# Performance work log

Hardware: AMD Instinct MI355X
Metric: run time of the kernel (lower is better)

Reference implementation:

```python
import jax, jax.numpy as jnp
import numpy as np

D_MODEL = 1024
NHEAD = 16
WINDOW = 128


def setup_inputs() -> dict:
    key = jax.random.key(0)
    ks = jax.random.split(key, 7)
    B, L, D = 4, 4096, D_MODEL
    s = 0.02
    return {
        "q": jax.random.normal(ks[0], (B, L, D), jnp.float32),
        "k": jax.random.normal(ks[1], (B, L, D), jnp.float32),
        "v": jax.random.normal(ks[2], (B, L, D), jnp.float32),
        "in_proj_w": jax.random.normal(ks[3], (3 * D, D), jnp.float32) * s,
        "in_proj_b": jnp.zeros((3 * D,), jnp.float32),
        "out_w": jax.random.normal(ks[4], (D, D), jnp.float32) * s,
        "out_b": jnp.zeros((D,), jnp.float32),
    }


def reference(q, k, v, in_proj_w, in_proj_b, out_w, out_b):
    B, L, D = q.shape
    H, W = NHEAD, WINDOW
    hd = D // H
    nW = L // W
    Wq, Wk, Wv = in_proj_w[:D], in_proj_w[D:2 * D], in_proj_w[2 * D:]
    bq, bk, bv = in_proj_b[:D], in_proj_b[D:2 * D], in_proj_b[2 * D:]
    # shared per-window projections (same weights every window, as in nn.MultiheadAttention)
    qp = (q @ Wq.T + bq).reshape(B, nW, W, H, hd)
    kp = (k @ Wk.T + bk).reshape(B, nW, W, H, hd)
    vp = (v @ Wv.T + bv).reshape(B, nW, W, H, hd)
    scale = 1.0 / np.sqrt(hd).astype(np.float32)
    # block-diagonal attention: scores only within each window n
    scores = jnp.einsum("bnqhd,bnkhd->bnhqk", qp, kp) * scale  # [B,nW,H,W,W]
    attn = jax.nn.softmax(scores, axis=-1)
    out = jnp.einsum("bnhqk,bnkhd->bnqhd", attn, vp).reshape(B, L, D)
    return out @ out_w.T + out_b
```

## Files before the change

kernel.cpp:

```cpp
#include <hip/hip_runtime.h>

#define M_TOK 16384
#define DM    1024

typedef __bf16 bf16x8 __attribute__((ext_vector_type(8)));
typedef float  f32x4  __attribute__((ext_vector_type(4)));
typedef unsigned short us8 __attribute__((ext_vector_type(8)));
typedef unsigned short us4 __attribute__((ext_vector_type(4)));

__device__ __forceinline__ unsigned short f2bf(float f) {
    unsigned u = __float_as_uint(f);
    u += 0x7FFFu + ((u >> 16) & 1u);
    return (unsigned short)(u >> 16);
}

__device__ __forceinline__ void gl2lds16(const unsigned short* g, unsigned short* l) {
    __builtin_amdgcn_global_load_lds(
        (const __attribute__((address_space(1))) unsigned int*)g,
        (__attribute__((address_space(3))) unsigned int*)l, 16, 0, 0);
}

__global__ __launch_bounds__(256) void conv_f2b(
    const float* __restrict__ src, unsigned short* __restrict__ dst, int n8)
{
    int i = blockIdx.x * blockDim.x + threadIdx.x;
    int stride = gridDim.x * blockDim.x;
    for (; i < n8; i += stride) {
        const float4* s = (const float4*)(src + (size_t)i * 8);
        float4 a = s[0], b = s[1];
        us8 o;
        o[0] = f2bf(a.x); o[1] = f2bf(a.y); o[2] = f2bf(a.z); o[3] = f2bf(a.w);
        o[4] = f2bf(b.x); o[5] = f2bf(b.y); o[6] = f2bf(b.z); o[7] = f2bf(b.w);
        *(us8*)(dst + (size_t)i * 8) = o;
    }
}

#define PIPE_WAIT8() asm volatile("s_waitcnt vmcnt(8)" ::: "memory")
#define PIPE_WAIT0() asm volatile("s_waitcnt vmcnt(0)" ::: "memory")

#define STAGE(G_, k0_, Lb_)                                                  \
    _Pragma("unroll")                                                        \
    for (int j = 0; j < 4; ++j) {                                            \
        int p = tid + j * 512;                                               \
        int kkp = p >> 10, rem = p & 1023;                                   \
        int r = rem >> 2, cp = rem & 3;                                      \
        int cl = cp ^ ((r >> 1) & 3);                                        \
        gl2lds16((G_) + (size_t)r * DM + (k0_) + kkp * 32 + cl * 8,          \
                 (Lb_) + p * 8);                                             \
    }

#define COMPUTE(bi_)                                                         \
    _Pragma("unroll")                                                        \
    for (int kk = 0; kk < 2; ++kk) {                                         \
        bf16x8 af[8], bb[4];                                                 \
        _Pragma("unroll")                                                    \
        for (int mi = 0; mi < 8; ++mi)                                       \
            af[mi] = *(const bf16x8*)(smem[bi_] + kk * 8192 + sA + mi * 512);\
        _Pragma("unroll")                                                    \
        for (int ni = 0; ni < 4; ++ni)                                       \
            bb[ni] = *(const bf16x8*)(smem[bi_] + kk * 8192 + sB + ni * 512);\
        __builtin_amdgcn_s_setprio(1);                                       \
        _Pragma("unroll")                                                    \
        for (int mi = 0; mi < 8; ++mi)                                       \
            _Pragma("unroll")                                                \
            for (int ni = 0; ni < 4; ++ni)                                   \
                acc[mi][ni] = __builtin_amdgcn_mfma_f32_16x16x32_bf16(       \
                    af[mi], bb[ni], acc[mi][ni], 0, 0, 0);                   \
        __builtin_amdgcn_s_setprio(0);                                       \
    }

#define GEMM256_CORE(A_, B_)                                                 \
    __shared__ unsigned short smem[2][32768];                    \
    const int tid = threadIdx.x, lane = tid & 63, wv = tid >> 6;             \
    const int wm = wv >> 2, wn = wv & 3;                                     \
    const int lrow = lane & 15, qd = lane >> 4;                              \
    const int orig = blockIdx.y * 4 + blockIdx.x;     \
    const int swz  = (orig & 7) * 32 + (orig >> 3);                          \
    const int mbase = (swz >> 2) * 256, nbase = (swz & 3) * 256;             \
    const unsigned short* Ab = (A_) + (size_t)mbase * DM;                    \
    const unsigned short* Bb = (B_) + (size_t)nbase * DM;                    \
              \
    const int sA = (qd ^ ((lrow >> 1) & 3)) * 8 + (wm * 128 + lrow) * 32;    \
    const int sB = (qd ^ ((lrow >> 1) & 3)) * 8 + (wn * 64 + lrow) * 32      \
                   + 16384;                                                  \
    f32x4 acc[8][4] = {};                                                    \
                                                \
    STAGE(Ab, 0, smem[0]);  STAGE(Bb, 0, smem[0] + 16384);                   \
    STAGE(Ab, 64, smem[1]); STAGE(Bb, 64, smem[1] + 16384);                  \
    PIPE_WAIT8();                                                            \
    __builtin_amdgcn_s_barrier();                                            \
    __builtin_amdgcn_sched_barrier(0);                                       \
    _Pragma("unroll 1")                                                      \
    for (int t = 0; t < 16; t += 2) {                                        \
        COMPUTE(0);                                                          \
        __builtin_amdgcn_sched_barrier(0);                                   \
        __builtin_amdgcn_s_barrier();       \
        if (t + 2 < 16) {                                                    \
            STAGE(Ab, (t + 2) * 64, smem[0]);                                \
            STAGE(Bb, (t + 2) * 64, smem[0] + 16384);                        \
            PIPE_WAIT8();                               \
        } else {                                                             \
            PIPE_WAIT0();                                    \
        }                                                                    \
        __builtin_amdgcn_s_barrier();                                        \
        __builtin_amdgcn_sched_barrier(0);                                   \
        COMPUTE(1);                                                          \
        __builtin_amdgcn_sched_barrier(0);                                   \
        __builtin_amdgcn_s_barrier();                                        \
        if (t + 3 < 16) {                                                    \
            STAGE(Ab, (t + 3) * 64, smem[1]);                                \
            STAGE(Bb, (t + 3) * 64, smem[1] + 16384);                        \
            PIPE_WAIT8();                               \
        } else if (t + 2 < 16) {                                             \
            PIPE_WAIT0();                                                    \
        }                                                                    \
        __builtin_amdgcn_s_barrier();                                        \
        __builtin_amdgcn_sched_barrier(0);                                   \
    }

__global__ __launch_bounds__(512, 2) void gemm256_qkv(
    const unsigned short* __restrict__ A, const unsigned short* __restrict__ W,
    const float* __restrict__ bias, unsigned short* __restrict__ C, int z)
{
    GEMM256_CORE(A, W)
    if (z <= 1) {
        #pragma unroll
        for (int ni = 0; ni < 4; ++ni) {
            int gc = nbase + wn * 64 + ni * 16 + lrow;
            int h = gc >> 6, dh = gc & 63;
            float bv = bias[gc];
            #pragma unroll
            for (int mi = 0; mi < 8; ++mi) {
                int gr0 = mbase + wm * 128 + mi * 16 + qd * 4;
                int b = gr0 >> 12;
                #pragma unroll
                for (int r = 0; r < 4; ++r) {
                    int tok = (gr0 + r) & 4095;
                    C[(((size_t)b * 16 + h) * 4096 + tok) * 64 + dh] =
                        f2bf(acc[mi][ni][r] + bv);
                }
            }
        }
    } else {
        #pragma unroll
        for (int ni = 0; ni < 4; ++ni) {
            int gc = nbase + wn * 64 + ni * 16 + lrow;
            int h = gc >> 6, dh = gc & 63;
            float bv = bias[gc];
            #pragma unroll
            for (int mi = 0; mi < 8; ++mi) {
                int gr0 = mbase + wm * 128 + mi * 16 + qd * 4;
                int b = gr0 >> 12, tok = gr0 & 4095;
                us4 pk;
                #pragma unroll
                for (int r = 0; r < 4; ++r) pk[r] = f2bf(acc[mi][ni][r] + bv);
                *(us4*)(C + (((size_t)b * 16 + h) * 64 + dh) * 4096 + tok) = pk;
            }
        }
    }
}

__global__ __launch_bounds__(512, 2) void gemm256_out(
    const unsigned short* __restrict__ A, const unsigned short* __restrict__ W,
    const float* __restrict__ bias, float* __restrict__ out)
{
    GEMM256_CORE(A, W)
    #pragma unroll
    for (int ni = 0; ni < 4; ++ni) {
        int gc = nbase + wn * 64 + ni * 16 + lrow;
        float bv = bias[gc];
        #pragma unroll
        for (int mi = 0; mi < 8; ++mi) {
            int gr0 = mbase + wm * 128 + mi * 16 + qd * 4;
            #pragma unroll
            for (int r = 0; r < 4; ++r)
                out[(size_t)(gr0 + r) * DM + gc] = acc[mi][ni][r] + bv;
        }
    }
}

__global__ __launch_bounds__(256) void attn_v2(
    const unsigned short* __restrict__ qh, const unsigned short* __restrict__ kh,
    const unsigned short* __restrict__ vt, unsigned short* __restrict__ aout)
{
    const int gid = blockIdx.x;
    const int h  = gid & 15;
    const int wi = (gid >> 4) & 31;
    const int b  = gid >> 9;
    const int bh = b * 16 + h;

    const unsigned short* Qp = qh + ((size_t)bh * 4096 + wi * 128) * 64;
    const unsigned short* Kp = kh + ((size_t)bh * 4096 + wi * 128) * 64;
    const unsigned short* Vp = vt + (size_t)bh * 64 * 4096 + wi * 128;

    const int tid = threadIdx.x, lane = tid & 63, wv = tid >> 6;
    const int lrow = lane & 15, qd = lane >> 4, kof = qd * 8;

    __shared__ unsigned short Ps[128 * 136];

    f32x4 acc[2][8] = {};
    #pragma unroll
    for (int ki = 0; ki < 2; ++ki) {
        bf16x8 a0 = *(const bf16x8*)(Qp + (wv * 32 +  0 + lrow) * 64 + ki * 32 + kof);
        bf16x8 a1 = *(const bf16x8*)(Qp + (wv * 32 + 16 + lrow) * 64 + ki * 32 + kof);
        #pragma unroll
        for (int ni = 0; ni < 8; ++ni) {
            bf16x8 bb = *(const bf16x8*)(Kp + (ni * 16 + lrow) * 64 + ki * 32 + kof);
            acc[0][ni] = __builtin_amdgcn_mfma_f32_16x16x32_bf16(a0, bb, acc[0][ni], 0, 0, 0);
            acc[1][ni] = __builtin_amdgcn_mfma_f32_16x16x32_bf16(a1, bb, acc[1][ni], 0, 0, 0);
        }
    }

    const float scale = 0.125f;
    #pragma unroll
    for (int mi = 0; mi < 2; ++mi) {
        #pragma unroll
        for (int r = 0; r < 4; ++r) {
            float sc[8];
            float mx = -3.4e38f;
            #pragma unroll
            for (int ni = 0; ni < 8; ++ni) { sc[ni] = acc[mi][ni][r] * scale; mx = fmaxf(mx, sc[ni]); }
            mx = fmaxf(mx, __shfl_xor(mx, 1));
            mx = fmaxf(mx, __shfl_xor(mx, 2));
            mx = fmaxf(mx, __shfl_xor(mx, 4));
            mx = fmaxf(mx, __shfl_xor(mx, 8));
            float sum = 0.f;
            #pragma unroll
            for (int ni = 0; ni < 8; ++ni) { sc[ni] = __expf(sc[ni] - mx); sum += sc[ni]; }
            sum += __shfl_xor(sum, 1);
            sum += __shfl_xor(sum, 2);
            sum += __shfl_xor(sum, 4);
            sum += __shfl_xor(sum, 8);
            float inv = 1.0f / sum;
            #pragma unroll
            for (int ni = 0; ni < 8; ++ni) acc[mi][ni][r] = sc[ni] * inv;
        }
    }

    #pragma unroll
    for (int mi = 0; mi < 2; ++mi)
        #pragma unroll
        for (int ni = 0; ni < 8; ++ni)
            #pragma unroll
            for (int r = 0; r < 4; ++r)
                Ps[(wv * 32 + mi * 16 + qd * 4 + r) * 136 + ni * 16 + lrow] =
                    f2bf(acc[mi][ni][r]);

    f32x4 o[2][4] = {};
    #pragma unroll
    for (int kj = 0; kj < 4; ++kj) {
        bf16x8 a0 = *(const bf16x8*)(Ps + (wv * 32 +  0 + lrow) * 136 + kj * 32 + kof);
        bf16x8 a1 = *(const bf16x8*)(Ps + (wv * 32 + 16 + lrow) * 136 + kj * 32 + kof);
        #pragma unroll
        for (int nd = 0; nd < 4; ++nd) {
            bf16x8 bb = *(const bf16x8*)(Vp + (size_t)(nd * 16 + lrow) * 4096 + kj * 32 + kof);
            o[0][nd] = __builtin_amdgcn_mfma_f32_16x16x32_bf16(a0, bb, o[0][nd], 0, 0, 0);
            o[1][nd] = __builtin_amdgcn_mfma_f32_16x16x32_bf16(a1, bb, o[1][nd], 0, 0, 0);
        }
    }

    #pragma unroll
    for (int mi = 0; mi < 2; ++mi)
        #pragma unroll
        for (int nd = 0; nd < 4; ++nd)
            #pragma unroll
            for (int r = 0; r < 4; ++r) {
                int R = wv * 32 + mi * 16 + qd * 4 + r;
                int c = h * 64 + nd * 16 + lrow;
                aout[(size_t)(b * 4096 + wi * 128 + R) * DM + c] = f2bf(o[mi][nd][r]);
            }
}

__global__ __launch_bounds__(256) void gemm_qkv_v1(
    const float* __restrict__ qin, const float* __restrict__ kin,
    const float* __restrict__ vin, const float* __restrict__ ipw,
    const float* __restrict__ ipb, unsigned short* __restrict__ qkv)
{
    __shared__ unsigned short As[128 * 40];
    __shared__ unsigned short Ws[128 * 40];
    const int z = blockIdx.z;
    const float* A  = (z == 0) ? qin : ((z == 1) ? kin : vin);
    const float* Wp = ipw + (size_t)z * DM * DM;
    const float* bp = ipb + z * DM;
    unsigned short* Cp = qkv + (size_t)z * M_TOK * DM;
    const int mbase = blockIdx.y * 128, nbase = blockIdx.x * 128;
    const int tid = threadIdx.x, lane = tid & 63, wv = tid >> 6;
    const int wrow = (wv >> 1) * 64, wcol = (wv & 1) * 64;
    const int lrow = lane & 15, kof = (lane >> 4) * 8;
    const int srow = tid >> 3, sc4 = tid & 7;
    f32x4 acc[4][4] = {};
    for (int ks = 0; ks < 32; ++ks) {
        const int k0 = ks * 32;
        __syncthreads();
        #pragma unroll
        for (int it = 0; it < 4; ++it) {
            int row = it * 32 + srow;
            float4 av = *(const float4*)(A  + (size_t)(mbase + row) * DM + k0 + sc4 * 4);
            float4 wf = *(const float4*)(Wp + (size_t)(nbase + row) * DM + k0 + sc4 * 4);
            us4 ap, wp4;
            ap[0] = f2bf(av.x); ap[1] = f2bf(av.y); ap[2] = f2bf(av.z); ap[3] = f2bf(av.w);
            wp4[0] = f2bf(wf.x); wp4[1] = f2bf(wf.y); wp4[2] = f2bf(wf.z); wp4[3] = f2bf(wf.w);
            *(us4*)(As + row * 40 + sc4 * 4) = ap;
            *(us4*)(Ws + row * 40 + sc4 * 4) = wp4;
        }
        __syncthreads();
        bf16x8 af[4], bfr[4];
        #pragma unroll
        for (int i = 0; i < 4; ++i) af[i]  = *(const bf16x8*)(As + (wrow + i * 16 + lrow) * 40 + kof);
        #pragma unroll
        for (int i = 0; i < 4; ++i) bfr[i] = *(const bf16x8*)(Ws + (wcol + i * 16 + lrow) * 40 + kof);
        #pragma unroll
        for (int i = 0; i < 4; ++i)
            #pragma unroll
            for (int j = 0; j < 4; ++j)
                acc[i][j] = __builtin_amdgcn_mfma_f32_16x16x32_bf16(af[i], bfr[j], acc[i][j], 0, 0, 0);
    }
    #pragma unroll
    for (int j = 0; j < 4; ++j) {
        int gc = nbase + wcol + j * 16 + lrow;
        float bv = bp[gc];
        #pragma unroll
        for (int i = 0; i < 4; ++i) {
            int gr0 = mbase + wrow + i * 16 + (lane >> 4) * 4;
            #pragma unroll
            for (int r = 0; r < 4; ++r)
                Cp[(size_t)(gr0 + r) * DM + gc] = f2bf(acc[i][j][r] + bv);
        }
    }
}

__global__ __launch_bounds__(256) void gemm_out_v1(
    const unsigned short* __restrict__ x, const float* __restrict__ ow,
    const float* __restrict__ ob, float* __restrict__ out)
{
    __shared__ unsigned short As[128 * 40];
    __shared__ unsigned short Ws[128 * 40];
    const int mbase = blockIdx.y * 128, nbase = blockIdx.x * 128;
    const int tid = threadIdx.x, lane = tid & 63, wv = tid >> 6;
    const int wrow = (wv >> 1) * 64, wcol = (wv & 1) * 64;
    const int lrow = lane & 15, kof = (lane >> 4) * 8;
    const int srow = tid >> 3, sc4 = tid & 7;
    f32x4 acc[4][4] = {};
    for (int ks = 0; ks < 32; ++ks) {
        const int k0 = ks * 32;
        __syncthreads();
        #pragma unroll
        for (int it = 0; it < 4; ++it) {
            int row = it * 32 + srow;
            us4 av = *(const us4*)(x + (size_t)(mbase + row) * DM + k0 + sc4 * 4);
            float4 wf = *(const float4*)(ow + (size_t)(nbase + row) * DM + k0 + sc4 * 4);
            us4 wp4;
            wp4[0] = f2bf(wf.x); wp4[1] = f2bf(wf.y); wp4[2] = f2bf(wf.z); wp4[3] = f2bf(wf.w);
            *(us4*)(As + row * 40 + sc4 * 4) = av;
            *(us4*)(Ws + row * 40 + sc4 * 4) = wp4;
        }
        __syncthreads();
        bf16x8 af[4], bfr[4];
        #pragma unroll
        for (int i = 0; i < 4; ++i) af[i]  = *(const bf16x8*)(As + (wrow + i * 16 + lrow) * 40 + kof);
        #pragma unroll
        for (int i = 0; i < 4; ++i) bfr[i] = *(const bf16x8*)(Ws + (wcol + i * 16 + lrow) * 40 + kof);
        #pragma unroll
        for (int i = 0; i < 4; ++i)
            #pragma unroll
            for (int j = 0; j < 4; ++j)
                acc[i][j] = __builtin_amdgcn_mfma_f32_16x16x32_bf16(af[i], bfr[j], acc[i][j], 0, 0, 0);
    }
    #pragma unroll
    for (int j = 0; j < 4; ++j) {
        int gc = nbase + wcol + j * 16 + lrow;
        float bv = ob[gc];
        #pragma unroll
        for (int i = 0; i < 4; ++i) {
            int gr0 = mbase + wrow + i * 16 + (lane >> 4) * 4;
            #pragma unroll
            for (int r = 0; r < 4; ++r)
                out[(size_t)(gr0 + r) * DM + gc] = acc[i][j][r] + bv;
        }
    }
}

__global__ __launch_bounds__(256) void attn_win_v1(
    const unsigned short* __restrict__ qkv, unsigned short* __restrict__ aout)
{
    const unsigned short* qp = qkv;
    const unsigned short* kp = qkv + (size_t)M_TOK * DM;
    const unsigned short* vp = qkv + 2 * (size_t)M_TOK * DM;
    const int gid = blockIdx.x;
    const int h = gid & 15, wi = (gid >> 4) & 31, b = gid >> 9;
    const size_t rowbase = (size_t)b * 4096 + (size_t)wi * 128;
    const int tid = threadIdx.x, lane = tid & 63, wv = tid >> 6;
    const int lrow = lane & 15, kof = (lane >> 4) * 8;
    __shared__ unsigned short sm[27136];
    unsigned short* Qs = sm;
    unsigned short* Ks = sm + 9216;
    unsigned short* Vt = sm + 18432;
    unsigned short* Ps = sm;
    {
        const int seg = tid & 7;
        #pragma unroll
        for (int it = 0; it < 4; ++it) {
            int r = it * 32 + (tid >> 3);
            size_t g = (rowbase + r) * DM + h * 64 + seg * 8;
            *(int4*)(Qs + r * 72 + seg * 8) = *(const int4*)(qp + g);
            *(int4*)(Ks + r * 72 + seg * 8) = *(const int4*)(kp + g);
        }
        #pragma unroll
        for (int it = 0; it < 4; ++it) {
            int j = tid & 127;
            int sg = it * 2 + (tid >> 7);
            us8 vv = *(const us8*)(vp + (rowbase + j) * DM + h * 64 + sg * 8);
            #pragma unroll
            for (int d = 0; d < 8; ++d) Vt[(sg * 8 + d) * 136 + j] = vv[d];
        }
    }
    __syncthreads();
    f32x4 acc[2][8] = {};
    #pragma unroll
    for (int ki = 0; ki < 2; ++ki) {
        bf16x8 a0 = *(const bf16x8*)(Qs + (wv * 32 +  0 + lrow) * 72 + ki * 32 + kof);
        bf16x8 a1 = *(const bf16x8*)(Qs + (wv * 32 + 16 + lrow) * 72 + ki * 32 + kof);
        #pragma unroll
        for (int ni = 0; ni < 8; ++ni) {
            bf16x8 bb = *(const bf16x8*)(Ks + (ni * 16 + lrow) * 72 + ki * 32 + kof);
            acc[0][ni] = __builtin_amdgcn_mfma_f32_16x16x32_bf16(a0, bb, acc[0][ni], 0, 0, 0);
            acc[1][ni] = __builtin_amdgcn_mfma_f32_16x16x32_bf16(a1, bb, acc[1][ni], 0, 0, 0);
        }
    }
    const float scale = 0.125f;
    #pragma unroll
    for (int mi = 0; mi < 2; ++mi) {
        #pragma unroll
        for (int r = 0; r < 4; ++r) {
            float sc[8];
            float mx = -3.4e38f;
            #pragma unroll
            for (int ni = 0; ni < 8; ++ni) { sc[ni] = acc[mi][ni][r] * scale; mx = fmaxf(mx, sc[ni]); }
            mx = fmaxf(mx, __shfl_xor(mx, 1)); mx = fmaxf(mx, __shfl_xor(mx, 2));
            mx = fmaxf(mx, __shfl_xor(mx, 4)); mx = fmaxf(mx, __shfl_xor(mx, 8));
            float sum = 0.f;
            #pragma unroll
            for (int ni = 0; ni < 8; ++ni) { sc[ni] = __expf(sc[ni] - mx); sum += sc[ni]; }
            sum += __shfl_xor(sum, 1); sum += __shfl_xor(sum, 2);
            sum += __shfl_xor(sum, 4); sum += __shfl_xor(sum, 8);
            float inv = 1.0f / sum;
            #pragma unroll
            for (int ni = 0; ni < 8; ++ni) acc[mi][ni][r] = sc[ni] * inv;
        }
    }
    __syncthreads();
    #pragma unroll
    for (int mi = 0; mi < 2; ++mi)
        #pragma unroll
        for (int ni = 0; ni < 8; ++ni)
            #pragma unroll
            for (int r = 0; r < 4; ++r)
                Ps[(wv * 32 + mi * 16 + (lane >> 4) * 4 + r) * 136 + ni * 16 + lrow] =
                    f2bf(acc[mi][ni][r]);
    __syncthreads();
    f32x4 o[2][4] = {};
    #pragma unroll
    for (int kj = 0; kj < 4; ++kj) {
        bf16x8 a0 = *(const bf16x8*)(Ps + (wv * 32 +  0 + lrow) * 136 + kj * 32 + kof);
        bf16x8 a1 = *(const bf16x8*)(Ps + (wv * 32 + 16 + lrow) * 136 + kj * 32 + kof);
        #pragma unroll
        for (int nd = 0; nd < 4; ++nd) {
            bf16x8 bb = *(const bf16x8*)(Vt + (nd * 16 + lrow) * 136 + kj * 32 + kof);
            o[0][nd] = __builtin_amdgcn_mfma_f32_16x16x32_bf16(a0, bb, o[0][nd], 0, 0, 0);
            o[1][nd] = __builtin_amdgcn_mfma_f32_16x16x32_bf16(a1, bb, o[1][nd], 0, 0, 0);
        }
    }
    #pragma unroll
    for (int mi = 0; mi < 2; ++mi)
        #pragma unroll
        for (int nd = 0; nd < 4; ++nd)
            #pragma unroll
            for (int r = 0; r < 4; ++r) {
                int R = wv * 32 + mi * 16 + (lane >> 4) * 4 + r;
                int c = h * 64 + nd * 16 + lrow;
                aout[(rowbase + R) * DM + c] = f2bf(o[mi][nd][r]);
            }
}

extern "C" void kernel_launch(void* const* d_in, const int* in_sizes, int n_in,
                              void* d_out, int out_size, void* d_ws, size_t ws_size,
                              hipStream_t stream) {
    const float* q   = (const float*)d_in[0];
    const float* k   = (const float*)d_in[1];
    const float* v   = (const float*)d_in[2];
    const float* ipw = (const float*)d_in[3];
    const float* ipb = (const float*)d_in[4];
    const float* ow  = (const float*)d_in[5];
    const float* ob  = (const float*)d_in[6];
    float* out = (float*)d_out;

    const size_t MD = (size_t)M_TOK * DM;
    const size_t WW = (size_t)DM * DM;
    const size_t need = (4 * MD + 3 * WW) * 2;

    if (ws_size >= need) {
        unsigned short* X   = (unsigned short*)d_ws;
        unsigned short* qh  = X + MD;
        unsigned short* kh  = X + 2 * MD;
        unsigned short* vtb = X + 3 * MD;
        unsigned short* Wb  = X + 4 * MD;
        unsigned short* aout = X;
        unsigned short* OwB  = Wb;

        conv_f2b<<<1536, 256, 0, stream>>>(ipw, Wb, (int)(3 * WW / 8));
        conv_f2b<<<8192, 256, 0, stream>>>(q, X, (int)(MD / 8));
        gemm256_qkv<<<dim3(4, 64), 512, 0, stream>>>(X, Wb, ipb, qh, 0);
        conv_f2b<<<8192, 256, 0, stream>>>(k, X, (int)(MD / 8));
        gemm256_qkv<<<dim3(4, 64), 512, 0, stream>>>(X, Wb + WW, ipb + DM, kh, 1);
        conv_f2b<<<8192, 256, 0, stream>>>(v, X, (int)(MD / 8));
        gemm256_qkv<<<dim3(4, 64), 512, 0, stream>>>(X, Wb + 2 * WW, ipb + 2 * DM, vtb, 2);
        conv_f2b<<<512, 256, 0, stream>>>(ow, OwB, (int)(WW / 8));
        attn_v2<<<2048, 256, 0, stream>>>(qh, kh, vtb, aout);
        gemm256_out<<<dim3(4, 64), 512, 0, stream>>>(aout, OwB, ob, out);
    } else {
        unsigned short* qkv = (unsigned short*)d_ws;
        const size_t qkv_elems = 3 * MD;
        const size_t need_full = (qkv_elems + MD) * 2;
        unsigned short* aout = (ws_size >= need_full) ? qkv + qkv_elems : qkv;
        gemm_qkv_v1<<<dim3(8, 128, 3), 256, 0, stream>>>(q, k, v, ipw, ipb, qkv);
        attn_win_v1<<<2048, 256, 0, stream>>>(qkv, aout);
        gemm_out_v1<<<dim3(8, 128), 256, 0, stream>>>(aout, ow, ob, out);
    }
}
```

Baseline: 531.9 us.

## Restructure GEMM LDS pipeline into 4-slot ring of 32-wide K stages

Replaces the double-buffered 64-wide K staging, which used two barriers per half-step, with a four-slot ring of 32-wide K slices. Each iteration issues loads two slices ahead and needs only one waitcnt plus one barrier. This should cut barrier count and keep more global-to-LDS loads in flight alongside the MFMA work. LDS use stays at 128KB. The tighter single-barrier scheme risks races, because the slot being written (kh+2) is the one read two iterations earlier.

```diff
diff --git a/kernel.cpp b/kernel.cpp
--- a/kernel.cpp
+++ b/kernel.cpp
@@ -35,30 +35,53 @@
     }
 }
 
-#define PIPE_WAIT8() asm volatile("s_waitcnt vmcnt(8)" ::: "memory")
-#define PIPE_WAIT0() asm volatile("s_waitcnt vmcnt(0)" ::: "memory")
-
-#define STAGE(G_, k0_, Lb_)                                                  \
-    _Pragma("unroll")                                                        \
-    for (int j = 0; j < 4; ++j) {                                            \
-        int p = tid + j * 512;                                               \
-        int kkp = p >> 10, rem = p & 1023;                                   \
-        int r = rem >> 2, cp = rem & 3;                                      \
-        int cl = cp ^ ((r >> 1) & 3);                                        \
-        gl2lds16((G_) + (size_t)r * DM + (k0_) + kkp * 32 + cl * 8,          \
-                 (Lb_) + p * 8);                                             \
-    }
-
-#define COMPUTE(bi_)                                                         \
-    _Pragma("unroll")                                                        \
-    for (int kk = 0; kk < 2; ++kk) {                                         \
+#define STAGE_HALF(x_)                                                       \
+    {                                                                        \
+        const int s_ = ((x_) & 3) * 8192;                                    \
+        _Pragma("unroll")                                                    \
+        for (int j = 0; j < 2; ++j) {                                        \
+            int p = tid + j * 512;                                           \
+            int r = p >> 2, cp = p & 3;                                      \
+            int cl = cp ^ ((r >> 1) & 3);                                    \
+            gl2lds16(Ab + (size_t)r * DM + (x_) * 32 + cl * 8,               \
+                     LA + s_ + p * 8);                                       \
+            gl2lds16(Bb + (size_t)r * DM + (x_) * 32 + cl * 8,               \
+                     LB + s_ + p * 8);                                       \
+        }                                                                    \
+    }
+
+#define GEMM256_CORE(A_, B_)                                                 \
+    __shared__ unsigned short smem[65536];                       \
+    const int tid = threadIdx.x, lane = tid & 63, wv = tid >> 6;             \
+    const int wm = wv >> 2, wn = wv & 3;                                     \
+    const int lrow = lane & 15, qd = lane >> 4;                              \
+    const int orig = blockIdx.y * 4 + blockIdx.x;     \
+    const int swz  = (orig & 7) * 32 + (orig >> 3);                          \
+    const int mbase = (swz >> 2) * 256, nbase = (swz & 3) * 256;             \
+    const unsigned short* Ab = (A_) + (size_t)mbase * DM;                    \
+    const unsigned short* Bb = (B_) + (size_t)nbase * DM;                    \
+    unsigned short* LA = smem;                                               \
+    unsigned short* LB = smem + 32768;                                       \
+    const int fsw  = (qd ^ ((lrow >> 1) & 3)) * 8;                           \
+    const int aoff = (wm * 128 + lrow) * 32 + fsw;                           \
+    const int boff = (wn * 64 + lrow) * 32 + fsw;                            \
+    f32x4 acc[8][4] = {};                                                    \
+    STAGE_HALF(0)                                                            \
+    STAGE_HALF(1)                                                            \
+    asm volatile("s_waitcnt vmcnt(4)" ::: "memory");                         \
+    __builtin_amdgcn_s_barrier();                                            \
+    __builtin_amdgcn_sched_barrier(0);                                       \
+    _Pragma("unroll 4")                                                      \
+    for (int kh = 0; kh < 32; ++kh) {                                        \
+        if (kh < 30) STAGE_HALF(kh + 2)                                      \
+        const int sb = (kh & 3) * 8192;                                      \
         bf16x8 af[8], bb[4];                                                 \
         _Pragma("unroll")                                                    \
         for (int mi = 0; mi < 8; ++mi)                                       \
-            af[mi] = *(const bf16x8*)(smem[bi_] + kk * 8192 + sA + mi * 512);\
+            af[mi] = *(const bf16x8*)(LA + sb + aoff + mi * 512);            \
         _Pragma("unroll")                                                    \
         for (int ni = 0; ni < 4; ++ni)                                       \
-            bb[ni] = *(const bf16x8*)(smem[bi_] + kk * 8192 + sB + ni * 512);\
+            bb[ni] = *(const bf16x8*)(LB + sb + boff + ni * 512);            \
         __builtin_amdgcn_s_setprio(1);                                       \
         _Pragma("unroll")                                                    \
         for (int mi = 0; mi < 8; ++mi)                                       \
@@ -67,53 +90,8 @@
                 acc[mi][ni] = __builtin_amdgcn_mfma_f32_16x16x32_bf16(       \
                     af[mi], bb[ni], acc[mi][ni], 0, 0, 0);                   \
         __builtin_amdgcn_s_setprio(0);                                       \
-    }
-
-#define GEMM256_CORE(A_, B_)                                                 \
-    __shared__ unsigned short smem[2][32768];                    \
-    const int tid = threadIdx.x, lane = tid & 63, wv = tid >> 6;             \
-    const int wm = wv >> 2, wn = wv & 3;                                     \
-    const int lrow = lane & 15, qd = lane >> 4;                              \
-    const int orig = blockIdx.y * 4 + blockIdx.x;     \
-    const int swz  = (orig & 7) * 32 + (orig >> 3);                          \
-    const int mbase = (swz >> 2) * 256, nbase = (swz & 3) * 256;             \
-    const unsigned short* Ab = (A_) + (size_t)mbase * DM;                    \
-    const unsigned short* Bb = (B_) + (size_t)nbase * DM;                    \
-              \
-    const int sA = (qd ^ ((lrow >> 1) & 3)) * 8 + (wm * 128 + lrow) * 32;    \
-    const int sB = (qd ^ ((lrow >> 1) & 3)) * 8 + (wn * 64 + lrow) * 32      \
-                   + 16384;                                                  \
-    f32x4 acc[8][4] = {};                                                    \
-                                                \
-    STAGE(Ab, 0, smem[0]);  STAGE(Bb, 0, smem[0] + 16384);                   \
-    STAGE(Ab, 64, smem[1]); STAGE(Bb, 64, smem[1] + 16384);                  \
-    PIPE_WAIT8();                                                            \
-    __builtin_amdgcn_s_barrier();                                            \
-    __builtin_amdgcn_sched_barrier(0);                                       \
-    _Pragma("unroll 1")                                                      \
-    for (int t = 0; t < 16; t += 2) {                                        \
-        COMPUTE(0);                                                          \
-        __builtin_amdgcn_sched_barrier(0);                                   \
-        __builtin_amdgcn_s_barrier();       \
-        if (t + 2 < 16) {                                                    \
-            STAGE(Ab, (t + 2) * 64, smem[0]);                                \
-            STAGE(Bb, (t + 2) * 64, smem[0] + 16384);                        \
-            PIPE_WAIT8();                               \
-        } else {                                                             \
-            PIPE_WAIT0();                                    \
-        }                                                                    \
-        __builtin_amdgcn_s_barrier();                                        \
-        __builtin_amdgcn_sched_barrier(0);                                   \
-        COMPUTE(1);                                                          \
-        __builtin_amdgcn_sched_barrier(0);                                   \
-        __builtin_amdgcn_s_barrier();                                        \
-        if (t + 3 < 16) {                                                    \
-            STAGE(Ab, (t + 3) * 64, smem[1]);                                \
-            STAGE(Bb, (t + 3) * 64, smem[1] + 16384);                        \
-            PIPE_WAIT8();                               \
-        } else if (t + 2 < 16) {                                             \
-            PIPE_WAIT0();                                                    \
-        }                                                                    \
+        if (kh < 30) { asm volatile("s_waitcnt vmcnt(4)" ::: "memory"); }    \
+        else         { asm volatile("s_waitcnt vmcnt(0)" ::: "memory"); }    \
         __builtin_amdgcn_s_barrier();                                        \
         __builtin_amdgcn_sched_barrier(0);                                   \
     }
```

Result: faster. 451.1 us (-15.2%).
